# Performance work log

Measured on AMD Instinct MI355X. Metric: run time of the kernel, lower is better.

Reference implementation:

```python
import jax, jax.numpy as jnp
import numpy as np

B, T, C = 4, 2048, 1024
H = 16
HS = C // H  # 64
FF = 4 * C
EPS = 1e-5


def setup_inputs() -> dict:
    key = jax.random.key(0)
    ks = jax.random.split(key, 12)
    s = lambda k, shape, fan: jax.random.normal(k, shape, jnp.float32) * (fan ** -0.5)
    return {
        "x": jax.random.normal(ks[0], (B, T, C), jnp.float32),
        "Wq": s(ks[1], (H, C, HS), C),
        "Wk": s(ks[2], (H, C, HS), C),
        "Wv": s(ks[3], (H, C, HS), C),
        "Wproj": s(ks[4], (C, C), C),
        "bproj": jnp.zeros((C,), jnp.float32),
        "W1": s(ks[5], (C, FF), C),
        "b1": jnp.zeros((FF,), jnp.float32),
        "W2": s(ks[6], (FF, C), FF),
        "b2": jnp.zeros((C,), jnp.float32),
        "g1": jnp.ones((C,), jnp.float32),
        "be1": jnp.zeros((C,), jnp.float32),
        "g2": jnp.ones((C,), jnp.float32),
        "be2": jnp.zeros((C,), jnp.float32),
    }


def _layernorm(x, g, b):
    mu = jnp.mean(x, axis=-1, keepdims=True)
    var = jnp.mean(jnp.square(x - mu), axis=-1, keepdims=True)
    return (x - mu) * jax.lax.rsqrt(var + EPS) * g + b


def reference(x, Wq, Wk, Wv, Wproj, bproj, W1, b1, W2, b2, g1, be1, g2, be2):
    # --- multi-head causal self-attention on ln1(x) ---
    h = _layernorm(x, g1, be1)                      # [B,T,C]
    q = jnp.einsum("btc,hcd->bhtd", h, Wq)
    k = jnp.einsum("btc,hcd->bhtd", h, Wk)
    v = jnp.einsum("btc,hcd->bhtd", h, Wv)
    scores = jnp.einsum("bhtd,bhsd->bhts", q, k) * (HS ** -0.5)  # [B,H,T,T]
    causal = jnp.tril(jnp.ones((T, T), bool))
    scores = jnp.where(causal, scores, -jnp.inf)
    wei = jax.nn.softmax(scores, axis=-1)
    attn = jnp.einsum("bhts,bhsd->bhtd", wei, v)    # [B,H,T,HS]
    attn = attn.transpose(0, 2, 1, 3).reshape(B, T, C)  # concat heads
    x = x + attn @ Wproj + bproj
    # --- feed-forward on ln2(x) ---
    h2 = _layernorm(x, g2, be2)
    x = x + jax.nn.relu(h2 @ W1 + b1) @ W2 + b2
    return x
```

## Files before the change

### kernel.cpp

```cpp
#include <hip/hip_runtime.h>
#include <hip/hip_bf16.h>
#include <stdint.h>


typedef unsigned short u16;
typedef __bf16 bf16x8 __attribute__((ext_vector_type(8)));
typedef float f32x4 __attribute__((ext_vector_type(4)));
typedef float f32x16 __attribute__((ext_vector_type(16)));

#define MFMA16(a, b, c) __builtin_amdgcn_mfma_f32_16x16x32_bf16((a), (b), (c), 0, 0, 0)
#define MFMA32(a, b, c) __builtin_amdgcn_mfma_f32_32x32x16_bf16((a), (b), (c), 0, 0, 0)

__device__ __forceinline__ u16 f2bf(float f) {
  __hip_bfloat16 h = __float2bfloat16(f);
  return __builtin_bit_cast(u16, h);
}

__device__ __forceinline__ uint32_t cvtpk(float lo, float hi_) {
  uint32_t r;
  asm("v_cvt_pk_bf16_f32 %0, %1, %2" : "=v"(r) : "v"(lo), "v"(hi_));
  return r;
}

__device__ __forceinline__ void pl32swap(uint32_t& a, uint32_t& b) {
  asm("v_permlane32_swap_b32 %0, %1" : "+v"(a), "+v"(b));
}

__device__ __forceinline__ void gload16(const void* g, void* l) {
  __builtin_amdgcn_global_load_lds(
      (__attribute__((address_space(1))) void*)g,
      (__attribute__((address_space(3))) void*)l, 16, 0, 0);
}

__global__ __launch_bounds__(256) void ln_kernel(
    const float* __restrict__ x, const float* __restrict__ g,
    const float* __restrict__ be, u16* __restrict__ out) {
  const int row = blockIdx.x;
  const int tid = threadIdx.x;
  const float4 v = reinterpret_cast<const float4*>(x + (size_t)row * 1024)[tid];
  float s = v.x + v.y + v.z + v.w;
  float s2 = v.x * v.x + v.y * v.y + v.z * v.z + v.w * v.w;
#pragma unroll
  for (int off = 1; off < 64; off <<= 1) {
    s += __shfl_xor(s, off);
    s2 += __shfl_xor(s2, off);
  }
  __shared__ float red[8];
  const int wid = tid >> 6;
  if ((tid & 63) == 0) { red[wid] = s; red[4 + wid] = s2; }
  __syncthreads();
  s = red[0] + red[1] + red[2] + red[3];
  s2 = red[4] + red[5] + red[6] + red[7];
  const float mu = s * (1.0f / 1024.0f);
  const float rstd = rsqrtf(s2 * (1.0f / 1024.0f) - mu * mu + 1e-5f);
  const float4 gv = reinterpret_cast<const float4*>(g)[tid];
  const float4 bv = reinterpret_cast<const float4*>(be)[tid];
  ushort4 o;
  o.x = f2bf((v.x - mu) * rstd * gv.x + bv.x);
  o.y = f2bf((v.y - mu) * rstd * gv.y + bv.y);
  o.z = f2bf((v.z - mu) * rstd * gv.z + bv.z);
  o.w = f2bf((v.w - mu) * rstd * gv.w + bv.w);
  *reinterpret_cast<ushort4*>(out + (size_t)row * 1024 + tid * 4) = o;
}

__global__ __launch_bounds__(256) void tcvt(
    const float* __restrict__ src, u16* __restrict__ dst,
    int R, int C, size_t sstride, size_t dstride) {
  src += (size_t)blockIdx.z * sstride;
  dst += (size_t)blockIdx.z * dstride;
  __shared__ float t[64][65];
  const int r0 = blockIdx.x * 64, c0 = blockIdx.y * 64;
  const int tid = threadIdx.x;
  const int cc = tid & 63, rr = tid >> 6;
#pragma unroll
  for (int p = 0; p < 16; ++p) {
    const int r = rr + p * 4;
    t[r][cc] = src[(size_t)(r0 + r) * C + c0 + cc];
  }
  __syncthreads();
#pragma unroll
  for (int p = 0; p < 16; ++p) {
    const int c = rr + p * 4;
    dst[(size_t)(c0 + c) * R + r0 + cc] = f2bf(t[cc][c]);
  }
}

constexpr int EPI_QKV = 0;
constexpr int EPI_RES = 1;
constexpr int EPI_RELU = 2;

template <int EPI>
__global__ __launch_bounds__(256) void gemm_bf16(
    const u16* __restrict__ A, const u16* __restrict__ Bt,
    int M, int N, int K,
    u16* outB, float* outF, const float* bias, const float* res) {
  __shared__ u16 sA[128 * 32] __attribute__((aligned(16)));
  __shared__ u16 sB[128 * 32] __attribute__((aligned(16)));
  const int tid = threadIdx.x;
  const int lane = tid & 63, wid = tid >> 6;
  const int bm = blockIdx.x, bn = blockIdx.y;
  const int wr = wid >> 1, wc = wid & 1;
  const int l16 = lane & 15, lg = lane >> 4;

  f32x4 acc[4][4];
#pragma unroll
  for (int m = 0; m < 4; ++m)
#pragma unroll
    for (int n = 0; n < 4; ++n) {
      acc[m][n][0] = 0.f; acc[m][n][1] = 0.f; acc[m][n][2] = 0.f; acc[m][n][3] = 0.f;
    }

  const size_t rowA = (size_t)bm * 128;
  const size_t rowB = (size_t)bn * 128;
  const int nkt = K >> 5;

  for (int kt = 0; kt < nkt; ++kt) {
    const int k0 = kt * 32;
#pragma unroll
    for (int it = 0; it < 2; ++it) {
      const int f = tid + it * 256;
      const int r = f >> 2;
      const int sl = (f & 3) ^ ((r >> 1) & 3);
      gload16(A + (rowA + r) * K + k0 + sl * 8, (char*)sA + wid * 1024 + it * 4096);
      gload16(Bt + (rowB + r) * K + k0 + sl * 8, (char*)sB + wid * 1024 + it * 4096);
    }
    __syncthreads();
    bf16x8 af[4], bfr[4];
#pragma unroll
    for (int m = 0; m < 4; ++m) {
      const int r = wr * 64 + m * 16 + l16;
      const int sl = lg ^ ((r >> 1) & 3);
      af[m] = *reinterpret_cast<const bf16x8*>(sA + r * 32 + sl * 8);
    }
#pragma unroll
    for (int n = 0; n < 4; ++n) {
      const int r = wc * 64 + n * 16 + l16;
      const int sl = lg ^ ((r >> 1) & 3);
      bfr[n] = *reinterpret_cast<const bf16x8*>(sB + r * 32 + sl * 8);
    }
#pragma unroll
    for (int m = 0; m < 4; ++m)
#pragma unroll
      for (int n = 0; n < 4; ++n)
        acc[m][n] = MFMA16(af[m], bfr[n], acc[m][n]);
    __syncthreads();
  }

#pragma unroll
  for (int m = 0; m < 4; ++m)
#pragma unroll
    for (int n = 0; n < 4; ++n)
#pragma unroll
      for (int ii = 0; ii < 4; ++ii) {
        const int gi = bm * 128 + wr * 64 + m * 16 + lg * 4 + ii;
        const int gj = bn * 128 + wc * 64 + n * 16 + l16;
        const float val = acc[m][n][ii];
        if constexpr (EPI == EPI_RES) {
          const size_t idx = (size_t)gi * N + gj;
          outF[idx] = val + bias[gj] + res[idx];
        } else {
          const float b = val + bias[gj];
          outB[(size_t)gi * N + gj] = f2bf(b > 0.f ? b : 0.f);
        }
      }
}

template <int EPI>
__global__ __launch_bounds__(512) void gemm256(
    const u16* __restrict__ A, const u16* __restrict__ Bt,
    int M, int N, int K, int NBN,
    u16* outB, float* outF, const float* bias) {
  __shared__ u16 sA[2][256 * 64] __attribute__((aligned(16)));
  __shared__ u16 sB[2][256 * 64] __attribute__((aligned(16)));
  const int tid = threadIdx.x;
  const int lane = tid & 63, wid = tid >> 6;
  const int wr = wid >> 2, wc = wid & 3;
  const int l16 = lane & 15, lg = lane >> 4;
  const int nwg = gridDim.x;
  const int wgid = (blockIdx.x & 7) * (nwg >> 3) + (blockIdx.x >> 3);
  const int bm = wgid / NBN, bn = wgid % NBN;
  const size_t rowA = (size_t)bm * 256;
  const size_t rowB = (size_t)bn * 256;
  const int nkt = K >> 6;

  f32x4 acc[8][4];
#pragma unroll
  for (int m = 0; m < 8; ++m)
#pragma unroll
    for (int n = 0; n < 4; ++n) {
      acc[m][n][0] = 0.f; acc[m][n][1] = 0.f; acc[m][n][2] = 0.f; acc[m][n][3] = 0.f;
    }

  auto stageA = [&](int kt, int h) {
    if (kt >= nkt) return;
    const int k0 = kt << 6;
    char* base = (char*)&sA[kt & 1][h * 8192];
#pragma unroll
    for (int it = 0; it < 2; ++it) {
      const int f = tid + it * 512;
      const int r = f >> 3, c = f & 7;
      gload16(A + (rowA + h * 128 + r) * K + k0 + ((c ^ (r & 7)) << 3), base + f * 16);
    }
  };
  auto stageB = [&](int kt, int h) {
    if (kt >= nkt) return;
    const int k0 = kt << 6;
    char* base = (char*)&sB[kt & 1][h * 8192];
#pragma unroll
    for (int it = 0; it < 2; ++it) {
      const int f = tid + it * 512;
      const int r = f >> 3, c = f & 7;
      gload16(Bt + (rowB + h * 128 + r) * K + k0 + ((c ^ (r & 7)) << 3), base + f * 16);
    }
  };

  stageA(0, 0); stageB(0, 0); stageA(0, 1); stageB(0, 1);
  stageB(1, 0); stageA(1, 0);
  asm volatile("s_waitcnt vmcnt(4)" ::: "memory");
  __builtin_amdgcn_s_barrier();
  asm volatile("" ::: "memory");

  bf16x8 a[4][2], b[4][2];
  for (int kt = 0; kt < nkt; ++kt) {
    const u16* bufA = &sA[kt & 1][0];
    const u16* bufB = &sB[kt & 1][0];
#pragma unroll
    for (int m = 0; m < 4; ++m)
#pragma unroll
      for (int kk = 0; kk < 2; ++kk) {
        const int r = wr * 128 + m * 16 + l16;
        a[m][kk] = *reinterpret_cast<const bf16x8*>(bufA + r * 64 + (((kk * 4 + lg) ^ (r & 7)) << 3));
      }
#pragma unroll
    for (int n = 0; n < 2; ++n)
#pragma unroll
      for (int kk = 0; kk < 2; ++kk) {
        const int r = wc * 64 + n * 16 + l16;
        b[n][kk] = *reinterpret_cast<const bf16x8*>(bufB + r * 64 + (((kk * 4 + lg) ^ (r & 7)) << 3));
      }
    stageB(kt + 1, 1);
    __builtin_amdgcn_s_barrier();
    asm volatile("s_waitcnt lgkmcnt(0)" ::: "memory");
    __builtin_amdgcn_s_setprio(1);
#pragma unroll
    for (int kk = 0; kk < 2; ++kk)
#pragma unroll
      for (int m = 0; m < 4; ++m)
#pragma unroll
        for (int n = 0; n < 2; ++n)
          acc[m][n] = MFMA16(a[m][kk], b[n][kk], acc[m][n]);
    __builtin_amdgcn_s_setprio(0);
    __builtin_amdgcn_s_barrier();
    asm volatile("" ::: "memory");
#pragma unroll
    for (int n = 2; n < 4; ++n)
#pragma unroll
      for (int kk = 0; kk < 2; ++kk) {
        const int r = wc * 64 + n * 16 + l16;
        b[n][kk] = *reinterpret_cast<const bf16x8*>(bufB + r * 64 + (((kk * 4 + lg) ^ (r & 7)) << 3));
      }
    stageA(kt + 1, 1);
    __builtin_amdgcn_s_barrier();
    asm volatile("s_waitcnt lgkmcnt(0)" ::: "memory");
    __builtin_amdgcn_s_setprio(1);
#pragma unroll
    for (int kk = 0; kk < 2; ++kk)
#pragma unroll
      for (int m = 0; m < 4; ++m)
#pragma unroll
        for (int n = 2; n < 4; ++n)
          acc[m][n] = MFMA16(a[m][kk], b[n][kk], acc[m][n]);
    __builtin_amdgcn_s_setprio(0);
    __builtin_amdgcn_s_barrier();
    asm volatile("" ::: "memory");
#pragma unroll
    for (int m = 0; m < 4; ++m)
#pragma unroll
      for (int kk = 0; kk < 2; ++kk) {
        const int r = wr * 128 + 64 + m * 16 + l16;
        a[m][kk] = *reinterpret_cast<const bf16x8*>(bufA + r * 64 + (((kk * 4 + lg) ^ (r & 7)) << 3));
      }
    stageB(kt + 2, 0);
    __builtin_amdgcn_s_barrier();
    asm volatile("s_waitcnt lgkmcnt(0)" ::: "memory");
    __builtin_amdgcn_s_setprio(1);
#pragma unroll
    for (int kk = 0; kk < 2; ++kk)
#pragma unroll
      for (int m = 0; m < 4; ++m)
#pragma unroll
        for (int n = 2; n < 4; ++n)
          acc[4 + m][n] = MFMA16(a[m][kk], b[n][kk], acc[4 + m][n]);
    __builtin_amdgcn_s_setprio(0);
    __builtin_amdgcn_s_barrier();
    asm volatile("" ::: "memory");
    stageA(kt + 2, 0);
    __builtin_amdgcn_s_setprio(1);
#pragma unroll
    for (int kk = 0; kk < 2; ++kk)
#pragma unroll
      for (int m = 0; m < 4; ++m)
#pragma unroll
        for (int n = 0; n < 2; ++n)
          acc[4 + m][n] = MFMA16(a[m][kk], b[n][kk], acc[4 + m][n]);
    __builtin_amdgcn_s_setprio(0);
    asm volatile("s_waitcnt vmcnt(4)" ::: "memory");
    __builtin_amdgcn_s_barrier();
    asm volatile("" ::: "memory");
  }

#pragma unroll
  for (int m = 0; m < 8; ++m)
#pragma unroll
    for (int n = 0; n < 4; ++n)
#pragma unroll
      for (int ii = 0; ii < 4; ++ii) {
        const int gi = bm * 256 + wr * 128 + m * 16 + lg * 4 + ii;
        const int gj = bn * 256 + wc * 64 + n * 16 + l16;
        const float val = acc[m][n][ii];
        if constexpr (EPI == EPI_QKV) {
          const int sel = gj >> 10;
          const int hh = (gj >> 6) & 15;
          const int dd = gj & 63;
          const int bb = gi >> 11, tt = gi & 2047;
          const float sv = (sel == 0) ? val * 0.1803368801f : val;
          outB[(size_t)sel * 8388608 + ((size_t)(bb * 16 + hh) * 2048 + tt) * 64 + dd] = f2bf(sv);
        } else {
          const float bv = val + bias[gj];
          outB[(size_t)gi * N + gj] = f2bf(bv > 0.f ? bv : 0.f);
        }
      }
}

__global__ __launch_bounds__(256, 3) void attn_kernel(
    const u16* __restrict__ q, const u16* __restrict__ k,
    const u16* __restrict__ v, u16* __restrict__ o) {
  const int bid = blockIdx.x;
  const int bh = (bid & 7) * 8 + ((bid >> 3) & 7);
  const int qt = 15 - (bid >> 6);
  const int tid = threadIdx.x;
  const int lane = tid & 63, wid = tid >> 6;
  const int l32 = lane & 31, hi = lane >> 5;
  const u16* qb = q + (size_t)bh * (2048 * 64);
  const u16* kb = k + (size_t)bh * (2048 * 64);
  const u16* vb = v + (size_t)bh * (2048 * 64);
  const int q0 = qt * 128;
  const int qrow = q0 + wid * 32 + l32;

  __shared__ u16 sK[2][64 * 64] __attribute__((aligned(16)));
  __shared__ u16 sVt[2][64 * 72] __attribute__((aligned(16)));

  bf16x8 bq[4];
#pragma unroll
  for (int s = 0; s < 4; ++s)
    bq[s] = *reinterpret_cast<const bf16x8*>(qb + (size_t)qrow * 64 + s * 16 + hi * 8);

  f32x16 oacc[2];
#pragma unroll
  for (int r = 0; r < 16; ++r) { oacc[0][r] = 0.f; oacc[1][r] = 0.f; }
  float mi = -1e30f, li = 0.f;

  uint4 vr0, vr1;

  auto stageK = [&](int s0, int buf) {
#pragma unroll
    for (int it = 0; it < 2; ++it) {
      const int f = tid + it * 256;
      const int r = f >> 3, c = f & 7;
      gload16(kb + (size_t)(s0 + r) * 64 + (size_t)((c ^ (r & 7)) * 8),
              (char*)&sK[buf][0] + it * 4096 + wid * 1024);
    }
  };
  auto loadV = [&](int s0) {
    const int kvp = tid & 31;
    const int c8 = tid >> 5;
    vr0 = *reinterpret_cast<const uint4*>(vb + (size_t)(s0 + 2 * kvp) * 64 + c8 * 8);
    vr1 = *reinterpret_cast<const uint4*>(vb + (size_t)(s0 + 2 * kvp + 1) * 64 + c8 * 8);
  };
  auto writeV = [&](int buf) {
    const int kvp = tid & 31;
    const int c8 = tid >> 5;
    const u16* e0 = reinterpret_cast<const u16*>(&vr0);
    const u16* e1 = reinterpret_cast<const u16*>(&vr1);
    u16* base = &sVt[buf][0];
#pragma unroll
    for (int j = 0; j < 8; ++j) {
      const int d = c8 * 8 + j;
      *reinterpret_cast<uint32_t*>(base + d * 72 + 2 * kvp) =
          (uint32_t)e0[j] | ((uint32_t)e1[j] << 16);
    }
  };

  const int nst = 2 * qt + 2;
  stageK(0, 0);
  loadV(0);
  asm volatile("s_waitcnt vmcnt(0)" ::: "memory");
  writeV(0);
  __syncthreads();

  int cur = 0;
  for (int ks = 0; ks < nst; ++ks) {
    const int s0 = ks * 64;
    const int nxt = cur ^ 1;
    if (ks + 1 < nst) { stageK(s0 + 64, nxt); loadV(s0 + 64); }

    f32x16 st[2];
#pragma unroll
    for (int r = 0; r < 16; ++r) { st[0][r] = 0.f; st[1][r] = 0.f; }
#pragma unroll
    for (int t = 0; t < 2; ++t) {
      const int row = t * 32 + l32;
      const int rx = row & 7;
#pragma unroll
      for (int s = 0; s < 4; ++s) {
        bf16x8 ak = *reinterpret_cast<const bf16x8*>(
            &sK[cur][0] + row * 64 + (((s * 2 + hi) ^ rx) << 3));
        st[t] = MFMA32(ak, bq[s], st[t]);
      }
    }

    if (ks >= 2 * qt) {
#pragma unroll
      for (int t = 0; t < 2; ++t)
#pragma unroll
        for (int a = 0; a < 4; ++a)
#pragma unroll
          for (int c2 = 0; c2 < 4; ++c2) {
            const int kvg = s0 + t * 32 + a * 8 + hi * 4 + c2;
            if (kvg > qrow) st[t][a * 4 + c2] = -1e30f;
          }
    }

    float pm = -3e38f;
#pragma unroll
    for (int t = 0; t < 2; ++t)
#pragma unroll
      for (int r = 0; r < 16; ++r) pm = fmaxf(pm, st[t][r]);
    pm = fmaxf(pm, __shfl_xor(pm, 32));
    if (__any(pm > mi)) {
      const float mn = fmaxf(mi, pm);
      const float al = exp2f(mi - mn);
      mi = mn;
      li *= al;
#pragma unroll
      for (int dt = 0; dt < 2; ++dt)
#pragma unroll
        for (int r = 0; r < 16; ++r) oacc[dt][r] *= al;
    }
    float rs = 0.f;
#pragma unroll
    for (int t = 0; t < 2; ++t)
#pragma unroll
      for (int r = 0; r < 16; ++r) {
        const float p = exp2f(st[t][r] - mi);
        st[t][r] = p;
        rs += p;
      }
    rs += __shfl_xor(rs, 32);
    li += rs;

    uint32_t W[2][4][2];
#pragma unroll
    for (int t = 0; t < 2; ++t)
#pragma unroll
      for (int a = 0; a < 4; ++a) {
        W[t][a][0] = cvtpk(st[t][a * 4 + 0], st[t][a * 4 + 1]);
        W[t][a][1] = cvtpk(st[t][a * 4 + 2], st[t][a * 4 + 3]);
      }
#pragma unroll
    for (int ks2 = 0; ks2 < 4; ++ks2) {
      const int t = ks2 >> 1;
      uint32_t A0 = W[t][(2 * ks2) & 3][0], B0 = W[t][(2 * ks2 + 1) & 3][0];
      uint32_t A1 = W[t][(2 * ks2) & 3][1], B1 = W[t][(2 * ks2 + 1) & 3][1];
      pl32swap(A0, B0);
      pl32swap(A1, B1);
      union { uint32_t w[4]; bf16x8 v; } bp;
      bp.w[0] = A0; bp.w[1] = A1; bp.w[2] = B0; bp.w[3] = B1;
#pragma unroll
      for (int dt = 0; dt < 2; ++dt) {
        bf16x8 av = *reinterpret_cast<const bf16x8*>(
            &sVt[cur][0] + (dt * 32 + l32) * 72 + ks2 * 16 + hi * 8);
        oacc[dt] = MFMA32(av, bp.v, oacc[dt]);
      }
    }

    if (ks + 1 < nst) {
      asm volatile("s_waitcnt vmcnt(0)" ::: "memory");
      writeV(nxt);
      __syncthreads();
    }
    cur = nxt;
  }

  const int bb = bh >> 4, hh = bh & 15;
  const float rli = 1.0f / li;
  const size_t rowo = (size_t)(bb * 2048 + qrow) * 1024;
#pragma unroll
  for (int dt = 0; dt < 2; ++dt)
#pragma unroll
    for (int a = 0; a < 4; ++a) {
      ushort4 pk;
      pk.x = f2bf(oacc[dt][a * 4 + 0] * rli);
      pk.y = f2bf(oacc[dt][a * 4 + 1] * rli);
      pk.z = f2bf(oacc[dt][a * 4 + 2] * rli);
      pk.w = f2bf(oacc[dt][a * 4 + 3] * rli);
      *reinterpret_cast<ushort4*>(o + rowo + hh * 64 + dt * 32 + a * 8 + hi * 4) = pk;
    }
}

extern "C" void kernel_launch(void* const* d_in, const int* in_sizes, int n_in,
                              void* d_out, int out_size, void* d_ws, size_t ws_size,
                              hipStream_t stream) {
  const float* x = (const float*)d_in[0];
  const float* Wq = (const float*)d_in[1];
  const float* Wk = (const float*)d_in[2];
  const float* Wv = (const float*)d_in[3];
  const float* Wproj = (const float*)d_in[4];
  const float* bproj = (const float*)d_in[5];
  const float* W1 = (const float*)d_in[6];
  const float* b1 = (const float*)d_in[7];
  const float* W2 = (const float*)d_in[8];
  const float* b2 = (const float*)d_in[9];
  const float* g1 = (const float*)d_in[10];
  const float* be1 = (const float*)d_in[11];
  const float* g2 = (const float*)d_in[12];
  const float* be2 = (const float*)d_in[13];
  float* out = (float*)d_out;

  char* ws = (char*)d_ws;
  const size_t MB16 = 16777216ull;
  u16* hb = (u16*)(ws);
  u16* qkv = (u16*)(ws + MB16);
  u16* qp = qkv;
  u16* kp = qkv + 8388608;
  u16* vp = qkv + 2 * 8388608;
  u16* ab = (u16*)(ws + 4 * MB16);
  u16* f1 = qkv;
  u16* wqkvt = (u16*)(ws + 5 * MB16);
  u16* wprojt = wqkvt + 3145728;
  u16* w1t = wprojt + 1048576;
  u16* w2t = w1t + 4194304;

  dim3 blk(256);
  tcvt<<<dim3(16, 1, 16), blk, 0, stream>>>(Wq, wqkvt, 1024, 64, 65536, 65536);
  tcvt<<<dim3(16, 1, 16), blk, 0, stream>>>(Wk, wqkvt + 1048576, 1024, 64, 65536, 65536);
  tcvt<<<dim3(16, 1, 16), blk, 0, stream>>>(Wv, wqkvt + 2097152, 1024, 64, 65536, 65536);
  tcvt<<<dim3(16, 16, 1), blk, 0, stream>>>(Wproj, wprojt, 1024, 1024, 0, 0);
  tcvt<<<dim3(16, 64, 1), blk, 0, stream>>>(W1, w1t, 1024, 4096, 0, 0);
  tcvt<<<dim3(64, 16, 1), blk, 0, stream>>>(W2, w2t, 4096, 1024, 0, 0);

  ln_kernel<<<8192, blk, 0, stream>>>(x, g1, be1, hb);
  gemm256<EPI_QKV><<<384, 512, 0, stream>>>(hb, wqkvt, 8192, 3072, 1024, 12,
                                            qkv, nullptr, nullptr);
  attn_kernel<<<1024, blk, 0, stream>>>(qp, kp, vp, ab);
  gemm_bf16<EPI_RES><<<dim3(64, 8), blk, 0, stream>>>(ab, wprojt, 8192, 1024, 1024,
                                                      nullptr, out, bproj, x);
  ln_kernel<<<8192, blk, 0, stream>>>(out, g2, be2, hb);
  gemm256<EPI_RELU><<<512, 512, 0, stream>>>(hb, w1t, 8192, 4096, 1024, 16,
                                             f1, nullptr, b1);
  gemm_bf16<EPI_RES><<<dim3(64, 8), blk, 0, stream>>>(f1, w2t, 8192, 1024, 4096,
                                                      nullptr, out, b2, out);
}
```

Measured before the change: 407.9 us.

## Replace simple 128x128 GEMM with pipelined 128x256 kernel for proj, FFN2, QKV

Adds a gemm128 kernel using 128x256 tiles, 512 threads, double-buffered LDS with swizzled async global loads and interleaved MFMA phases. It replaces the unpipelined single-buffer gemm_bf16 for the output projection and second FFN GEMM, and the QKV GEMM now uses it with 768 blocks instead of 384 large tiles for better CU fill. It also drains outstanding loads with vmcnt(0) on the final iterations. The main risks are higher register and LDS use, and the smaller QKV tile reusing each loaded operand less.

```diff
diff --git a/kernel.cpp b/kernel.cpp
--- a/kernel.cpp
+++ b/kernel.cpp
@@ -90,82 +90,6 @@
 constexpr int EPI_RELU = 2;
 
 template <int EPI>
-__global__ __launch_bounds__(256) void gemm_bf16(
-    const u16* __restrict__ A, const u16* __restrict__ Bt,
-    int M, int N, int K,
-    u16* outB, float* outF, const float* bias, const float* res) {
-  __shared__ u16 sA[128 * 32] __attribute__((aligned(16)));
-  __shared__ u16 sB[128 * 32] __attribute__((aligned(16)));
-  const int tid = threadIdx.x;
-  const int lane = tid & 63, wid = tid >> 6;
-  const int bm = blockIdx.x, bn = blockIdx.y;
-  const int wr = wid >> 1, wc = wid & 1;
-  const int l16 = lane & 15, lg = lane >> 4;
-
-  f32x4 acc[4][4];
-#pragma unroll
-  for (int m = 0; m < 4; ++m)
-#pragma unroll
-    for (int n = 0; n < 4; ++n) {
-      acc[m][n][0] = 0.f; acc[m][n][1] = 0.f; acc[m][n][2] = 0.f; acc[m][n][3] = 0.f;
-    }
-
-  const size_t rowA = (size_t)bm * 128;
-  const size_t rowB = (size_t)bn * 128;
-  const int nkt = K >> 5;
-
-  for (int kt = 0; kt < nkt; ++kt) {
-    const int k0 = kt * 32;
-#pragma unroll
-    for (int it = 0; it < 2; ++it) {
-      const int f = tid + it * 256;
-      const int r = f >> 2;
-      const int sl = (f & 3) ^ ((r >> 1) & 3);
-      gload16(A + (rowA + r) * K + k0 + sl * 8, (char*)sA + wid * 1024 + it * 4096);
-      gload16(Bt + (rowB + r) * K + k0 + sl * 8, (char*)sB + wid * 1024 + it * 4096);
-    }
-    __syncthreads();
-    bf16x8 af[4], bfr[4];
-#pragma unroll
-    for (int m = 0; m < 4; ++m) {
-      const int r = wr * 64 + m * 16 + l16;
-      const int sl = lg ^ ((r >> 1) & 3);
-      af[m] = *reinterpret_cast<const bf16x8*>(sA + r * 32 + sl * 8);
-    }
-#pragma unroll
-    for (int n = 0; n < 4; ++n) {
-      const int r = wc * 64 + n * 16 + l16;
-      const int sl = lg ^ ((r >> 1) & 3);
-      bfr[n] = *reinterpret_cast<const bf16x8*>(sB + r * 32 + sl * 8);
-    }
-#pragma unroll
-    for (int m = 0; m < 4; ++m)
-#pragma unroll
-      for (int n = 0; n < 4; ++n)
-        acc[m][n] = MFMA16(af[m], bfr[n], acc[m][n]);
-    __syncthreads();
-  }
-
-#pragma unroll
-  for (int m = 0; m < 4; ++m)
-#pragma unroll
-    for (int n = 0; n < 4; ++n)
-#pragma unroll
-      for (int ii = 0; ii < 4; ++ii) {
-        const int gi = bm * 128 + wr * 64 + m * 16 + lg * 4 + ii;
-        const int gj = bn * 128 + wc * 64 + n * 16 + l16;
-        const float val = acc[m][n][ii];
-        if constexpr (EPI == EPI_RES) {
-          const size_t idx = (size_t)gi * N + gj;
-          outF[idx] = val + bias[gj] + res[idx];
-        } else {
-          const float b = val + bias[gj];
-          outB[(size_t)gi * N + gj] = f2bf(b > 0.f ? b : 0.f);
-        }
-      }
-}
-
-template <int EPI>
 __global__ __launch_bounds__(512) void gemm256(
     const u16* __restrict__ A, const u16* __restrict__ Bt,
     int M, int N, int K, int NBN,
@@ -304,7 +228,11 @@
         for (int n = 0; n < 2; ++n)
           acc[4 + m][n] = MFMA16(a[m][kk], b[n][kk], acc[4 + m][n]);
     __builtin_amdgcn_s_setprio(0);
-    asm volatile("s_waitcnt vmcnt(4)" ::: "memory");
+    if (kt + 2 < nkt) {
+      asm volatile("s_waitcnt vmcnt(4)" ::: "memory");
+    } else {
+      asm volatile("s_waitcnt vmcnt(0)" ::: "memory");
+    }
     __builtin_amdgcn_s_barrier();
     asm volatile("" ::: "memory");
   }
@@ -316,6 +244,166 @@
 #pragma unroll
       for (int ii = 0; ii < 4; ++ii) {
         const int gi = bm * 256 + wr * 128 + m * 16 + lg * 4 + ii;
+        const int gj = bn * 256 + wc * 64 + n * 16 + l16;
+        const float val = acc[m][n][ii];
+        if constexpr (EPI == EPI_RELU) {
+          const float bv = val + bias[gj];
+          outB[(size_t)gi * N + gj] = f2bf(bv > 0.f ? bv : 0.f);
+        }
+      }
+}
+
+template <int EPI>
+__global__ __launch_bounds__(512) void gemm128(
+    const u16* __restrict__ A, const u16* __restrict__ Bt,
+    int M, int N, int K, int NBN,
+    u16* outB, float* outF, const float* bias, const float* res) {
+  __shared__ u16 sA[2][128 * 64] __attribute__((aligned(16)));
+  __shared__ u16 sB[2][256 * 64] __attribute__((aligned(16)));
+  const int tid = threadIdx.x;
+  const int lane = tid & 63, wid = tid >> 6;
+  const int wr = wid >> 2, wc = wid & 3;
+  const int l16 = lane & 15, lg = lane >> 4;
+  const int nwg = gridDim.x;
+  const int wgid = (blockIdx.x & 7) * (nwg >> 3) + (blockIdx.x >> 3);
+  const int bm = wgid / NBN, bn = wgid % NBN;
+  const size_t rowA = (size_t)bm * 128;
+  const size_t rowB = (size_t)bn * 256;
+  const int nkt = K >> 6;
+
+  f32x4 acc[4][4];
+#pragma unroll
+  for (int m = 0; m < 4; ++m)
+#pragma unroll
+    for (int n = 0; n < 4; ++n) {
+      acc[m][n][0] = 0.f; acc[m][n][1] = 0.f; acc[m][n][2] = 0.f; acc[m][n][3] = 0.f;
+    }
+
+  auto stageA = [&](int kt, int h) {
+    if (kt >= nkt) return;
+    const int k0 = kt << 6;
+    char* base = (char*)&sA[kt & 1][h * 4096];
+    const int r = tid >> 3, c = tid & 7;
+    gload16(A + (rowA + h * 64 + r) * K + k0 + ((c ^ (r & 7)) << 3), base + tid * 16);
+  };
+  auto stageB = [&](int kt, int h) {
+    if (kt >= nkt) return;
+    const int k0 = kt << 6;
+    char* base = (char*)&sB[kt & 1][h * 8192];
+#pragma unroll
+    for (int it = 0; it < 2; ++it) {
+      const int f = tid + it * 512;
+      const int r = f >> 3, c = f & 7;
+      gload16(Bt + (rowB + h * 128 + r) * K + k0 + ((c ^ (r & 7)) << 3), base + f * 16);
+    }
+  };
+
+  stageA(0, 0); stageB(0, 0); stageA(0, 1); stageB(0, 1);
+  stageB(1, 0); stageA(1, 0);
+  asm volatile("s_waitcnt vmcnt(3)" ::: "memory");
+  __builtin_amdgcn_s_barrier();
+  asm volatile("" ::: "memory");
+
+  bf16x8 a[2][2], b[4][2];
+  for (int kt = 0; kt < nkt; ++kt) {
+    const u16* bufA = &sA[kt & 1][0];
+    const u16* bufB = &sB[kt & 1][0];
+#pragma unroll
+    for (int m = 0; m < 2; ++m)
+#pragma unroll
+      for (int kk = 0; kk < 2; ++kk) {
+        const int r = wr * 64 + m * 16 + l16;
+        a[m][kk] = *reinterpret_cast<const bf16x8*>(bufA + r * 64 + (((kk * 4 + lg) ^ (r & 7)) << 3));
+      }
+#pragma unroll
+    for (int n = 0; n < 2; ++n)
+#pragma unroll
+      for (int kk = 0; kk < 2; ++kk) {
+        const int r = wc * 64 + n * 16 + l16;
+        b[n][kk] = *reinterpret_cast<const bf16x8*>(bufB + r * 64 + (((kk * 4 + lg) ^ (r & 7)) << 3));
+      }
+    stageB(kt + 1, 1);
+    __builtin_amdgcn_s_barrier();
+    asm volatile("s_waitcnt lgkmcnt(0)" ::: "memory");
+    __builtin_amdgcn_s_setprio(1);
+#pragma unroll
+    for (int kk = 0; kk < 2; ++kk)
+#pragma unroll
+      for (int m = 0; m < 2; ++m)
+#pragma unroll
+        for (int n = 0; n < 2; ++n)
+          acc[m][n] = MFMA16(a[m][kk], b[n][kk], acc[m][n]);
+    __builtin_amdgcn_s_setprio(0);
+    __builtin_amdgcn_s_barrier();
+    asm volatile("" ::: "memory");
+#pragma unroll
+    for (int n = 2; n < 4; ++n)
+#pragma unroll
+      for (int kk = 0; kk < 2; ++kk) {
+        const int r = wc * 64 + n * 16 + l16;
+        b[n][kk] = *reinterpret_cast<const bf16x8*>(bufB + r * 64 + (((kk * 4 + lg) ^ (r & 7)) << 3));
+      }
+    stageA(kt + 1, 1);
+    __builtin_amdgcn_s_barrier();
+    asm volatile("s_waitcnt lgkmcnt(0)" ::: "memory");
+    __builtin_amdgcn_s_setprio(1);
+#pragma unroll
+    for (int kk = 0; kk < 2; ++kk)
+#pragma unroll
+      for (int m = 0; m < 2; ++m)
+#pragma unroll
+        for (int n = 2; n < 4; ++n)
+          acc[m][n] = MFMA16(a[m][kk], b[n][kk], acc[m][n]);
+    __builtin_amdgcn_s_setprio(0);
+    __builtin_amdgcn_s_barrier();
+    asm volatile("" ::: "memory");
+#pragma unroll
+    for (int m = 0; m < 2; ++m)
+#pragma unroll
+      for (int kk = 0; kk < 2; ++kk) {
+        const int r = wr * 64 + (m + 2) * 16 + l16;
+        a[m][kk] = *reinterpret_cast<const bf16x8*>(bufA + r * 64 + (((kk * 4 + lg) ^ (r & 7)) << 3));
+      }
+    stageB(kt + 2, 0);
+    __builtin_amdgcn_s_barrier();
+    asm volatile("s_waitcnt lgkmcnt(0)" ::: "memory");
+    __builtin_amdgcn_s_setprio(1);
+#pragma unroll
+    for (int kk = 0; kk < 2; ++kk)
+#pragma unroll
+      for (int m = 0; m < 2; ++m)
+#pragma unroll
+        for (int n = 2; n < 4; ++n)
+          acc[2 + m][n] = MFMA16(a[m][kk], b[n][kk], acc[2 + m][n]);
+    __builtin_amdgcn_s_setprio(0);
+    __builtin_amdgcn_s_barrier();
+    asm volatile("" ::: "memory");
+    stageA(kt + 2, 0);
+    __builtin_amdgcn_s_setprio(1);
+#pragma unroll
+    for (int kk = 0; kk < 2; ++kk)
+#pragma unroll
+      for (int m = 0; m < 2; ++m)
+#pragma unroll
+        for (int n = 0; n < 2; ++n)
+          acc[2 + m][n] = MFMA16(a[m][kk], b[n][kk], acc[2 + m][n]);
+    __builtin_amdgcn_s_setprio(0);
+    if (kt + 2 < nkt) {
+      asm volatile("s_waitcnt vmcnt(3)" ::: "memory");
+    } else {
+      asm volatile("s_waitcnt vmcnt(0)" ::: "memory");
+    }
+    __builtin_amdgcn_s_barrier();
+    asm volatile("" ::: "memory");
+  }
+
+#pragma unroll
+  for (int m = 0; m < 4; ++m)
+#pragma unroll
+    for (int n = 0; n < 4; ++n)
+#pragma unroll
+      for (int ii = 0; ii < 4; ++ii) {
+        const int gi = bm * 128 + wr * 64 + m * 16 + lg * 4 + ii;
         const int gj = bn * 256 + wc * 64 + n * 16 + l16;
         const float val = acc[m][n][ii];
         if constexpr (EPI == EPI_QKV) {
@@ -325,9 +413,9 @@
           const int bb = gi >> 11, tt = gi & 2047;
           const float sv = (sel == 0) ? val * 0.1803368801f : val;
           outB[(size_t)sel * 8388608 + ((size_t)(bb * 16 + hh) * 2048 + tt) * 64 + dd] = f2bf(sv);
-        } else {
-          const float bv = val + bias[gj];
-          outB[(size_t)gi * N + gj] = f2bf(bv > 0.f ? bv : 0.f);
+        } else if constexpr (EPI == EPI_RES) {
+          const size_t idx = (size_t)gi * N + gj;
+          outF[idx] = val + bias[gj] + res[idx];
         }
       }
 }
@@ -550,14 +638,14 @@
   tcvt<<<dim3(64, 16, 1), blk, 0, stream>>>(W2, w2t, 4096, 1024, 0, 0);
 
   ln_kernel<<<8192, blk, 0, stream>>>(x, g1, be1, hb);
-  gemm256<EPI_QKV><<<384, 512, 0, stream>>>(hb, wqkvt, 8192, 3072, 1024, 12,
-                                            qkv, nullptr, nullptr);
+  gemm128<EPI_QKV><<<768, 512, 0, stream>>>(hb, wqkvt, 8192, 3072, 1024, 12,
+                                            qkv, nullptr, nullptr, nullptr);
   attn_kernel<<<1024, blk, 0, stream>>>(qp, kp, vp, ab);
-  gemm_bf16<EPI_RES><<<dim3(64, 8), blk, 0, stream>>>(ab, wprojt, 8192, 1024, 1024,
-                                                      nullptr, out, bproj, x);
+  gemm128<EPI_RES><<<256, 512, 0, stream>>>(ab, wprojt, 8192, 1024, 1024, 4,
+                                            nullptr, out, bproj, x);
   ln_kernel<<<8192, blk, 0, stream>>>(out, g2, be2, hb);
   gemm256<EPI_RELU><<<512, 512, 0, stream>>>(hb, w1t, 8192, 4096, 1024, 16,
                                              f1, nullptr, b1);
-  gemm_bf16<EPI_RES><<<dim3(64, 8), blk, 0, stream>>>(f1, w2t, 8192, 1024, 4096,
-                                                      nullptr, out, b2, out);
-}
+  gemm128<EPI_RES><<<256, 512, 0, stream>>>(f1, w2t, 8192, 1024, 4096, 4,
+                                            nullptr, out, b2, out);
+}
```

After: 407.1 us. About the same (-0.2%).
